# Optimization experiments

Hardware: AMD Instinct MI355X
Metric: run time of the kernel (lower is better)

The kernel has to match this reference:

```python
import jax, jax.numpy as jnp
import numpy as np

N_NODES = 10000
N_EDGES = 50000
IN_F = 1433
OUT_F = 256
EPSILON = 8.0
SENSITIVITY = 1.0
DELTA = 1e-5
# total noise = sum of 3 independent per-share Gaussian draws
SIGMA = np.sqrt(3.0) * np.sqrt(2.0 * np.log(1.25 / DELTA)) * SENSITIVITY / EPSILON


def setup_inputs() -> dict:
    key = jax.random.key(0)
    k1, k2, k3, k4, k5, k6 = jax.random.split(key, 6)
    input_features = jax.random.normal(k1, (N_NODES, IN_F), dtype=jnp.float32)
    dst = jax.random.randint(k2, (N_EDGES,), 0, N_NODES)
    # src in [0, N_NODES]; value == N_NODES is the zero-vector sentinel
    src = jax.random.randint(k3, (N_EDGES,), 0, N_NODES + 1)
    edges = jnp.stack([dst, src], axis=1).astype(jnp.int64)
    stdv = 1.0 / np.sqrt(OUT_F)
    weight = jax.random.uniform(k4, (IN_F, OUT_F), minval=-stdv, maxval=stdv, dtype=jnp.float32)
    bias = jax.random.uniform(k5, (OUT_F,), minval=-stdv, maxval=stdv, dtype=jnp.float32)
    noise = jax.random.normal(k6, (N_NODES, IN_F), dtype=jnp.float32) * jnp.float32(SIGMA)
    return {"input_features": input_features, "edges": edges, "weight": weight,
            "bias": bias, "noise": noise}


def reference(input_features, edges, weight, bias, noise):
    n = input_features.shape[0]
    dst = edges[:, 0]
    src = edges[:, 1]
    # gather per-edge source features; sentinel src == n -> zero vector
    valid = (src < n)[:, None]                                   # [E,1]
    gathered = jnp.where(valid, input_features[jnp.clip(src, 0, n - 1)], 0.0)  # [E,F]
    # three secret shares sum exactly back to the value; the per-key aggregation
    # of each share then summed equals a single segment-sum over destinations
    agg = jax.ops.segment_sum(gathered, dst, num_segments=n)      # [N,F]
    # DP noise added to each share -> total noise added to the sum
    agg = agg + noise
    # torch.nn.functional.normalize(p=2, dim=1) with eps=1e-12
    norm = jnp.maximum(jnp.linalg.norm(agg, axis=1, keepdims=True), 1e-12)
    normed = agg / norm
    return normed @ weight + bias
```

## Files before the change

### kernel.cpp

```cpp
#include <hip/hip_runtime.h>
#include <math.h>

#define N_NODES 10000
#define N_EDGES 50000
#define IN_F    1433
#define OUT_F   256
#define GK      1440
#define NCHUNK  180
#define GM2     10112
#define CAP     32

typedef __bf16 bf16x8 __attribute__((ext_vector_type(8)));
typedef float  f32x4  __attribute__((ext_vector_type(4)));

typedef __attribute__((address_space(3))) unsigned int lds_u32;
typedef __attribute__((address_space(1))) unsigned int glb_u32;

__device__ __forceinline__ void stage16(const void* g, void* l) {
    __builtin_amdgcn_global_load_lds((glb_u32*)g, (lds_u32*)l, 16, 0, 0);
}


#define FILL_BLKS   ((N_EDGES + 255) / 256)
#define CONV_BLKS   (N_NODES / 4)
#define PREP_BLKS   (GK / 16)
#define PHASEA_BLKS (FILL_BLKS + CONV_BLKS + PREP_BLKS)

__global__ void __launch_bounds__(256) k_phaseA(const float* __restrict__ X,
                                                __bf16* __restrict__ Xbf,
                                                const float* __restrict__ W,
                                                __bf16* __restrict__ BT,
                                                const int* __restrict__ edges,
                                                int* __restrict__ cnt,
                                                int* __restrict__ slots,
                                                int* __restrict__ ovf) {
    __shared__ float wt[16][256];
    const int t = threadIdx.x;
    const int b = blockIdx.x;

    if (b < FILL_BLKS) {
        int e = b * 256 + t;
        if (e < N_EDGES) {
            int dst = edges[2 * e];
            int src = edges[2 * e + 1];
            if ((unsigned)src < N_NODES) {
                int pos = atomicAdd(&cnt[dst], 1);
                if (pos < CAP) {
                    slots[dst * CAP + pos] = src;
                } else {
                    int o = atomicAdd(&cnt[N_NODES], 1);
                    ovf[2 * o]     = dst;
                    ovf[2 * o + 1] = src;
                }
            }
        }
        return;
    }

    if (b < FILL_BLKS + CONV_BLKS) {
        const int w = t >> 6, lane = t & 63;
        const int r = (b - FILL_BLKS) * 4 + w;
        const size_t rowf = (size_t)r * IN_F;
        __bf16* orow = Xbf + (size_t)r * GK;
        const int d = r & 3;

        f32x4 A[3][3];
#pragma unroll
        for (int s2 = 0; s2 < 3; ++s2) {
            int k = lane + s2 * 64;
            int kc = (k > 178) ? 178 : k;
            size_t q0 = (rowf + (size_t)kc * 8) >> 2;
            A[s2][0] = ((const f32x4*)X)[q0];
            A[s2][1] = ((const f32x4*)X)[q0 + 1];
            A[s2][2] = ((const f32x4*)X)[q0 + 2];
        }

#pragma unroll
        for (int s2 = 0; s2 < 3; ++s2) {
            int k = lane + s2 * 64;
            float q[12];
            *(f32x4*)&q[0] = A[s2][0];
            *(f32x4*)&q[4] = A[s2][1];
            *(f32x4*)&q[8] = A[s2][2];
            if (k < 179) {
                bf16x8 v;
                switch (d) {
                case 0:
#pragma unroll
                    for (int j = 0; j < 8; ++j) v[j] = (__bf16)q[0 + j];
                    break;
                case 1:
#pragma unroll
                    for (int j = 0; j < 8; ++j) v[j] = (__bf16)q[1 + j];
                    break;
                case 2:
#pragma unroll
                    for (int j = 0; j < 8; ++j) v[j] = (__bf16)q[2 + j];
                    break;
                default:
#pragma unroll
                    for (int j = 0; j < 8; ++j) v[j] = (__bf16)q[3 + j];
                    break;
                }
                *(bf16x8*)(orow + k * 8) = v;
            } else if (k == 179) {
                bf16x8 v;
                v[0] = (__bf16)q[8 + d];
#pragma unroll
                for (int j = 1; j < 8; ++j) v[j] = (__bf16)0.0f;
                *(bf16x8*)(orow + 1432) = v;
            }
        }
        return;
    }

    {
        const int bp = b - FILL_BLKS - CONV_BLKS;
        const int k0 = bp * 16;
#pragma unroll
        for (int g2 = 0; g2 < 4; ++g2) {
            int g = t + g2 * 256;
            int r = g >> 6, c4 = g & 63;
            int krow = k0 + r;
            f32x4 v = (krow < IN_F)
                        ? ((const f32x4*)(W + (size_t)krow * OUT_F))[c4]
                        : (f32x4){0.f, 0.f, 0.f, 0.f};
            *(f32x4*)&wt[r][c4 * 4] = v;
        }
        __syncthreads();
        bf16x8 o0, o1;
#pragma unroll
        for (int r = 0; r < 8; ++r) { o0[r] = (__bf16)wt[r][t]; o1[r] = (__bf16)wt[8 + r][t]; }
        *(bf16x8*)(BT + (size_t)t * GK + k0)     = o0;
        *(bf16x8*)(BT + (size_t)t * GK + k0 + 8) = o1;
    }
}


__global__ void __launch_bounds__(192) k_agg(const __bf16* __restrict__ Xbf,
                                             const float* __restrict__ noise,
                                             const int* __restrict__ cnt,
                                             const int* __restrict__ slots,
                                             const int* __restrict__ ovf,
                                             __bf16* __restrict__ aggbf,
                                             float* __restrict__ rnorm) {
    __shared__ float red[3];
    const int node = blockIdx.x;
    const int t = threadIdx.x;
    const bool active = (t < NCHUNK);
    const size_t co = (size_t)t * 8;

    if (node >= N_NODES) {
        if (active) {
            bf16x8 z;
#pragma unroll
            for (int j = 0; j < 8; ++j) z[j] = (__bf16)0.0f;
            *(bf16x8*)(aggbf + (size_t)node * GK + co) = z;
        }
        return;
    }

    const size_t nrowf = (size_t)node * IN_F;
    const int d = node & 3;
    f32x4 na, nb, nc;
    if (active) {
        int kc = (t > 178) ? 178 : t;
        size_t q0 = (nrowf + (size_t)kc * 8) >> 2;
        na = ((const f32x4*)noise)[q0];
        nb = ((const f32x4*)noise)[q0 + 1];
        nc = ((const f32x4*)noise)[q0 + 2];
    }

    const int cn = cnt[node];
    const int ns = (cn < CAP) ? cn : CAP;
    const int* sl = slots + node * CAP;

    float acc[8] = {0.f, 0.f, 0.f, 0.f, 0.f, 0.f, 0.f, 0.f};

    int kk = 0;
    for (; kk + 3 < ns; kk += 4) {
        int n0 = sl[kk], n1 = sl[kk + 1];
        int n2 = sl[kk + 2], n3 = sl[kk + 3];
        if (active) {
            bf16x8 v0 = *(const bf16x8*)(Xbf + (size_t)n0 * GK + co);
            bf16x8 v1 = *(const bf16x8*)(Xbf + (size_t)n1 * GK + co);
            bf16x8 v2 = *(const bf16x8*)(Xbf + (size_t)n2 * GK + co);
            bf16x8 v3 = *(const bf16x8*)(Xbf + (size_t)n3 * GK + co);
#pragma unroll
            for (int j = 0; j < 8; ++j)
                acc[j] += ((float)v0[j] + (float)v1[j]) + ((float)v2[j] + (float)v3[j]);
        }
    }
    for (; kk < ns; ++kk) {
        int n0 = sl[kk];
        if (active) {
            bf16x8 v = *(const bf16x8*)(Xbf + (size_t)n0 * GK + co);
#pragma unroll
            for (int j = 0; j < 8; ++j) acc[j] += (float)v[j];
        }
    }

    if (cn > CAP) {
        const int L = cnt[N_NODES];
        for (int i = 0; i < L; ++i) {
            if (ovf[2 * i] == node) {
                int n0 = ovf[2 * i + 1];
                if (active) {
                    bf16x8 v = *(const bf16x8*)(Xbf + (size_t)n0 * GK + co);
#pragma unroll
                    for (int j = 0; j < 8; ++j) acc[j] += (float)v[j];
                }
            }
        }
    }

    if (active) {
        float nq[12];
        *(f32x4*)&nq[0] = na; *(f32x4*)&nq[4] = nb; *(f32x4*)&nq[8] = nc;
        if (t < 179) {
            switch (d) {
            case 0:
#pragma unroll
                for (int j = 0; j < 8; ++j) acc[j] += nq[0 + j];
                break;
            case 1:
#pragma unroll
                for (int j = 0; j < 8; ++j) acc[j] += nq[1 + j];
                break;
            case 2:
#pragma unroll
                for (int j = 0; j < 8; ++j) acc[j] += nq[2 + j];
                break;
            default:
#pragma unroll
                for (int j = 0; j < 8; ++j) acc[j] += nq[3 + j];
                break;
            }
        } else {
            acc[0] += nq[8 + d];
        }
    }

    float ss = 0.f;
    if (active) {
        bf16x8 o;
#pragma unroll
        for (int j = 0; j < 8; ++j) { o[j] = (__bf16)acc[j]; ss += acc[j] * acc[j]; }
        *(bf16x8*)(aggbf + (size_t)node * GK + co) = o;
    }
    for (int off = 32; off > 0; off >>= 1) ss += __shfl_down(ss, off, 64);
    if ((t & 63) == 0) red[t >> 6] = ss;
    __syncthreads();
    if (t == 0)
        rnorm[node] = 1.0f / fmaxf(sqrtf(red[0] + red[1] + red[2]), 1e-12f);
}


#define BKG 96
#define GEMM_NWG ((GM2 / 64) * (OUT_F / 64))

__global__ void __launch_bounds__(256) k_gemm(const __bf16* __restrict__ A,
                                              const __bf16* __restrict__ BT,
                                              const float* __restrict__ rnorm,
                                              const float* __restrict__ bias,
                                              float* __restrict__ out) {
    __shared__ __align__(16) __bf16 Asm[64][BKG];
    __shared__ __align__(16) __bf16 Bsm[64][BKG];

    const int t = threadIdx.x;
    const int lane = t & 63;
    const int w = t >> 6;
    const int wr = w >> 1, wc = w & 1;

    const int L = blockIdx.x;
    const int xcd = L & 7, idx = L >> 3;
    const int work = xcd * (GEMM_NWG / 8) + idx;
    const int row0 = (work >> 2) * 64;
    const int col0 = (work & 3) * 64;

    f32x4 acc[2][2];
#pragma unroll
    for (int i = 0; i < 2; ++i)
#pragma unroll
        for (int j = 0; j < 2; ++j) acc[i][j] = (f32x4){0.f, 0.f, 0.f, 0.f};

    __bf16* asm0 = (__bf16*)Asm;
    __bf16* bsm0 = (__bf16*)Bsm;

    auto stage_tile = [&](int k0) {
#pragma unroll
        for (int g2 = 0; g2 < 3; ++g2) {
            int g = t + g2 * 256;
            int r = g / 12, c16 = g % 12;
            stage16(A  + (size_t)(row0 + r) * GK + k0 + c16 * 8, asm0 + g * 8);
            stage16(BT + (size_t)(col0 + r) * GK + k0 + c16 * 8, bsm0 + g * 8);
        }
    };

    stage_tile(0);

    const int kq = (lane >> 4) * 8;
    const int l15 = lane & 15;

    for (int kt = 0; kt < GK / BKG; ++kt) {
        __syncthreads();

        bf16x8 af[2][3], bfr[2][3];
#pragma unroll
        for (int s = 0; s < 3; ++s) {
#pragma unroll
            for (int i = 0; i < 2; ++i) {
                af[i][s]  = *(const bf16x8*)&Asm[wr * 32 + i * 16 + l15][s * 32 + kq];
                bfr[i][s] = *(const bf16x8*)&Bsm[wc * 32 + i * 16 + l15][s * 32 + kq];
            }
        }

        __syncthreads();

        if (kt + 1 < GK / BKG) stage_tile((kt + 1) * BKG);

#pragma unroll
        for (int s = 0; s < 3; ++s)
#pragma unroll
            for (int i = 0; i < 2; ++i)
#pragma unroll
                for (int j = 0; j < 2; ++j)
                    acc[i][j] = __builtin_amdgcn_mfma_f32_16x16x32_bf16(af[i][s], bfr[j][s], acc[i][j], 0, 0, 0);
    }

    const int rq4 = (lane >> 4) * 4;
#pragma unroll
    for (int i = 0; i < 2; ++i) {
        int gr0 = row0 + wr * 32 + i * 16 + rq4;
#pragma unroll
        for (int rr = 0; rr < 4; ++rr) {
            int gr = gr0 + rr;
            if (gr < N_NODES) {
                float rn = rnorm[gr];
#pragma unroll
                for (int j = 0; j < 2; ++j) {
                    int gc = col0 + wc * 32 + j * 16 + l15;
                    out[(size_t)gr * OUT_F + gc] = acc[i][j][rr] * rn + bias[gc];
                }
            }
        }
    }
}


extern "C" void kernel_launch(void* const* d_in, const int* in_sizes, int n_in,
                              void* d_out, int out_size, void* d_ws, size_t ws_size,
                              hipStream_t stream) {
    const float* feat  = (const float*)d_in[0];
    const int*   edges = (const int*)d_in[1];
    const float* W     = (const float*)d_in[2];
    const float* bias  = (const float*)d_in[3];
    const float* noise = (const float*)d_in[4];
    float* out = (float*)d_out;

    char* ws = (char*)d_ws;
    size_t off = 0;
    auto carve = [&](size_t bytes) {
        void* p = ws + off;
        off = (off + bytes + 255) & ~(size_t)255;
        return p;
    };
    __bf16* Xbf     = (__bf16*)carve((size_t)N_NODES * GK * sizeof(__bf16));
    __bf16* aggbf   = (__bf16*)carve((size_t)GM2 * GK * sizeof(__bf16));
    __bf16* WbfT    = (__bf16*)carve((size_t)OUT_F * GK * sizeof(__bf16));
    float*  rnorm   = (float*)carve((size_t)N_NODES * sizeof(float));
    int*    cnt     = (int*)carve((size_t)(N_NODES + 1) * sizeof(int));
    int*    slots   = (int*)carve((size_t)N_NODES * CAP * sizeof(int));
    int*    ovf     = (int*)carve((size_t)2 * N_EDGES * sizeof(int));
    (void)ws_size;

    hipMemsetAsync(cnt, 0, (size_t)(N_NODES + 1) * sizeof(int), stream);

    k_phaseA<<<PHASEA_BLKS, 256, 0, stream>>>(feat, Xbf, W, WbfT,
                                              edges, cnt, slots, ovf);

    k_agg<<<GM2, 192, 0, stream>>>(Xbf, noise, cnt, slots, ovf, aggbf, rnorm);

    k_gemm<<<GEMM_NWG, 256, 0, stream>>>(aggbf, WbfT, rnorm, bias, out);
}
```

Measured before the change: 184.0 us.

## Double-buffer LDS tiles in the GEMM and use nontemporal output stores

Splits the GEMM's A and B shared-memory tiles into two buffers. The next K-tile's global-to-LDS load is issued before the current tile is read and fed to MFMA, which overlaps the fetch with compute and drops one barrier per iteration. Per-thread staging addresses are now computed once before the loop, and the fp32 output is written with nontemporal stores. The cost is twice the LDS per block, which may lower occupancy, and the GEMM is likely only a small part of the total pipeline time.

```diff
diff --git a/kernel.cpp b/kernel.cpp
--- a/kernel.cpp
+++ b/kernel.cpp
@@ -257,6 +257,7 @@
 
 
 #define BKG 96
+#define NKT (GK / BKG)
 #define GEMM_NWG ((GM2 / 64) * (OUT_F / 64))
 
 __global__ void __launch_bounds__(256) k_gemm(const __bf16* __restrict__ A,
@@ -264,8 +265,8 @@
                                               const float* __restrict__ rnorm,
                                               const float* __restrict__ bias,
                                               float* __restrict__ out) {
-    __shared__ __align__(16) __bf16 Asm[64][BKG];
-    __shared__ __align__(16) __bf16 Bsm[64][BKG];
+    __shared__ __align__(16) __bf16 Asm[2][64][BKG];
+    __shared__ __align__(16) __bf16 Bsm[2][64][BKG];
 
     const int t = threadIdx.x;
     const int lane = t & 63;
@@ -284,40 +285,46 @@
 #pragma unroll
         for (int j = 0; j < 2; ++j) acc[i][j] = (f32x4){0.f, 0.f, 0.f, 0.f};
 
-    __bf16* asm0 = (__bf16*)Asm;
-    __bf16* bsm0 = (__bf16*)Bsm;
-
-    auto stage_tile = [&](int k0) {
+    const __bf16* Ab[3];
+    const __bf16* Bb[3];
+    int goff[3];
+#pragma unroll
+    for (int g2 = 0; g2 < 3; ++g2) {
+        int g = t + g2 * 256;
+        int r = g / 12, c16 = g % 12;
+        Ab[g2]   = A  + (size_t)(row0 + r) * GK + c16 * 8;
+        Bb[g2]   = BT + (size_t)(col0 + r) * GK + c16 * 8;
+        goff[g2] = g * 8;
+    }
+
+    auto stage_tile = [&](int buf, int k0) {
 #pragma unroll
         for (int g2 = 0; g2 < 3; ++g2) {
-            int g = t + g2 * 256;
-            int r = g / 12, c16 = g % 12;
-            stage16(A  + (size_t)(row0 + r) * GK + k0 + c16 * 8, asm0 + g * 8);
-            stage16(BT + (size_t)(col0 + r) * GK + k0 + c16 * 8, bsm0 + g * 8);
+            stage16(Ab[g2] + k0, (__bf16*)Asm[buf] + goff[g2]);
+            stage16(Bb[g2] + k0, (__bf16*)Bsm[buf] + goff[g2]);
         }
     };
 
-    stage_tile(0);
+    stage_tile(0, 0);
 
     const int kq = (lane >> 4) * 8;
     const int l15 = lane & 15;
 
-    for (int kt = 0; kt < GK / BKG; ++kt) {
-        __syncthreads();
+    __syncthreads();
+
+    for (int kt = 0; kt < NKT; ++kt) {
+        const int cur = kt & 1;
+        if (kt + 1 < NKT) stage_tile(cur ^ 1, (kt + 1) * BKG);
 
         bf16x8 af[2][3], bfr[2][3];
 #pragma unroll
         for (int s = 0; s < 3; ++s) {
 #pragma unroll
             for (int i = 0; i < 2; ++i) {
-                af[i][s]  = *(const bf16x8*)&Asm[wr * 32 + i * 16 + l15][s * 32 + kq];
-                bfr[i][s] = *(const bf16x8*)&Bsm[wc * 32 + i * 16 + l15][s * 32 + kq];
-            }
-        }
-
-        __syncthreads();
-
-        if (kt + 1 < GK / BKG) stage_tile((kt + 1) * BKG);
+                af[i][s]  = *(const bf16x8*)&Asm[cur][wr * 32 + i * 16 + l15][s * 32 + kq];
+                bfr[i][s] = *(const bf16x8*)&Bsm[cur][wc * 32 + i * 16 + l15][s * 32 + kq];
+            }
+        }
 
 #pragma unroll
         for (int s = 0; s < 3; ++s)
@@ -326,6 +333,8 @@
 #pragma unroll
                 for (int j = 0; j < 2; ++j)
                     acc[i][j] = __builtin_amdgcn_mfma_f32_16x16x32_bf16(af[i][s], bfr[j][s], acc[i][j], 0, 0, 0);
+
+        __syncthreads();
     }
 
     const int rq4 = (lane >> 4) * 4;
@@ -340,7 +349,8 @@
 #pragma unroll
                 for (int j = 0; j < 2; ++j) {
                     int gc = col0 + wc * 32 + j * 16 + l15;
-                    out[(size_t)gr * OUT_F + gc] = acc[i][j][rr] * rn + bias[gc];
+                    __builtin_nontemporal_store(acc[i][j][rr] * rn + bias[gc],
+                                                &out[(size_t)gr * OUT_F + gc]);
                 }
             }
         }
```

New measurement: 188.1 us. 2.2% more time.
